# Performance work log

Hardware: AMD Instinct MI355X
Metric: run time of the kernel (lower is better)

The kernel has to match this reference:

```python
import jax, jax.numpy as jnp
import numpy as np

NUM_EXPERTS = 8
TOP_K = 2
HIDDEN = 1024
NUM_TOKENS = 8192


def setup_inputs() -> dict:
    key = jax.random.key(0)
    k1, k2, k3 = jax.random.split(key, 3)
    x = jax.random.normal(k1, (NUM_TOKENS, HIDDEN), dtype=jnp.float32)
    # gate: nn.Linear(hidden, num_experts, bias=False) -> weight [E, H]
    gate_w = jax.random.normal(k2, (NUM_EXPERTS, HIDDEN), dtype=jnp.float32) * 0.02
    # experts: nn.Linear(hidden, hidden, bias=False) stacked -> [E, H_out, H_in]
    expert_w = jax.random.normal(k3, (NUM_EXPERTS, HIDDEN, HIDDEN), dtype=jnp.float32) * 0.02
    return {"x": x, "gate_w": gate_w, "expert_w": expert_w}


def reference(x, gate_w, expert_w):
    # --- routing ---
    logits = jnp.einsum("th,eh->te", x, gate_w)          # [T, E]
    probs = jax.nn.softmax(logits, axis=-1)
    weights, indices = jax.lax.top_k(probs, TOP_K)        # [T, K], [T, K]

    # --- expert compute (equivalent of dispatch + per-expert GEMM) ---
    # y_e = x @ W_e^T for every expert; tokens then gather their top-k rows.
    all_y = jnp.einsum("td,ehd->eth", x, expert_w)        # [E, T, H]

    # --- weighted combine (gather by routed expert ids) ---
    t_idx = jnp.arange(x.shape[0])[None, :]               # [1, T]
    y_sel = all_y[indices.T, t_idx, :]                    # [K, T, H]
    out = jnp.einsum("tk,kth->th", weights, y_sel)        # [T, H]
    return out
```

## Files before the change

### kernel.cpp

```cpp
#include <hip/hip_runtime.h>
#include <hip/hip_bf16.h>
#include <stdint.h>

#define NUM_TOKENS 8192
#define HIDDEN 1024
#define NEXP 8
#define TOPK 2

typedef __bf16 bf16;
typedef __bf16 bf16x4 __attribute__((ext_vector_type(4)));
typedef __bf16 bf16x8 __attribute__((ext_vector_type(8)));
typedef float f32x4 __attribute__((ext_vector_type(4)));

__device__ __forceinline__ void gld_lds16(const void* g, void* l) {
  __builtin_amdgcn_global_load_lds(
      (const __attribute__((address_space(1))) void*)(uintptr_t)g,
      (__attribute__((address_space(3))) void*)(uint32_t)(uintptr_t)l,
      16, 0, 0);
}

__global__ __launch_bounds__(256) void gate_route_kernel(
    const float* __restrict__ x, const float* __restrict__ gw,
    bf16* __restrict__ xbf, int* __restrict__ echoice, float* __restrict__ pchoice)
{
  const int wid  = threadIdx.x >> 6;
  const int lane = threadIdx.x & 63;
  const int t = blockIdx.x * 4 + wid;

  const float* xrow = x + (size_t)t * HIDDEN;
  bf16* xbrow = xbf + (size_t)t * HIDDEN;

  float acc[NEXP];
#pragma unroll
  for (int e = 0; e < NEXP; ++e) acc[e] = 0.f;

#pragma unroll
  for (int it = 0; it < 4; ++it) {
    const int idx = it * 256 + lane * 4;
    float4 xv = *(const float4*)(xrow + idx);
    bf16x4 xb;
    xb[0] = (bf16)xv.x; xb[1] = (bf16)xv.y; xb[2] = (bf16)xv.z; xb[3] = (bf16)xv.w;
    *(bf16x4*)(xbrow + idx) = xb;
#pragma unroll
    for (int e = 0; e < NEXP; ++e) {
      float4 gv = *(const float4*)(gw + e * HIDDEN + idx);
      acc[e] += xv.x * gv.x + xv.y * gv.y + xv.z * gv.z + xv.w * gv.w;
    }
  }
#pragma unroll
  for (int e = 0; e < NEXP; ++e) {
#pragma unroll
    for (int off = 32; off > 0; off >>= 1)
      acc[e] += __shfl_xor(acc[e], off, 64);
  }

  if (lane == 0) {
    float m = acc[0];
#pragma unroll
    for (int e = 1; e < NEXP; ++e) m = fmaxf(m, acc[e]);
    float p[NEXP]; float s = 0.f;
#pragma unroll
    for (int e = 0; e < NEXP; ++e) { p[e] = expf(acc[e] - m); s += p[e]; }
    const float inv = 1.f / s;
#pragma unroll
    for (int e = 0; e < NEXP; ++e) p[e] *= inv;
    int i0 = 0; float p0 = p[0];
#pragma unroll
    for (int e = 1; e < NEXP; ++e) if (p[e] > p0) { p0 = p[e]; i0 = e; }
    int i1 = -1; float p1 = -1.f;
#pragma unroll
    for (int e = 0; e < NEXP; ++e) if (e != i0 && p[e] > p1) { p1 = p[e]; i1 = e; }

    echoice[t]              = i0;
    echoice[NUM_TOKENS + t] = i1;
    pchoice[t]              = p0;
    pchoice[NUM_TOKENS + t] = p1;
  }
}

__global__ __launch_bounds__(1024) void build_lists_kernel(
    const int* __restrict__ echoice, const float* __restrict__ pchoice,
    int* __restrict__ cnt, int* __restrict__ tok, float* __restrict__ wt)
{
  const int tid  = threadIdx.x;
  const int wave = tid >> 6;
  const int lane = tid & 63;
  const int k = wave >> 3;
  const int w = wave & 7;
  const int tbase = w * 1024;

  const int*   ec = echoice + k * NUM_TOKENS;
  const float* pc = pchoice + k * NUM_TOKENS;

  __shared__ int wcnt[2][8][NEXP];
  __shared__ int woff[2][8][NEXP];

  const unsigned long long lower = ((unsigned long long)1 << lane) - 1;

  int   ev[16];
  float pv[16];
#pragma unroll
  for (int c = 0; c < 16; ++c) {
    ev[c] = ec[tbase + c * 64 + lane];
    pv[c] = pc[tbase + c * 64 + lane];
  }

  int cl[NEXP];
#pragma unroll
  for (int e = 0; e < NEXP; ++e) cl[e] = 0;
#pragma unroll
  for (int c = 0; c < 16; ++c) {
#pragma unroll
    for (int l = 0; l < NEXP; ++l)
      cl[l] += __popcll(__ballot(ev[c] == l));
  }
  if (lane < NEXP) wcnt[k][w][lane] = cl[lane];
  __syncthreads();

  if (lane < NEXP) {
    int off = 0;
#pragma unroll
    for (int ww = 0; ww < 8; ++ww) {
      if (ww == w) woff[k][w][lane] = off;
      off += wcnt[k][ww][lane];
    }
    if (w == 0) cnt[k * NEXP + lane] = off;
  }
  __syncthreads();

  int run[NEXP];
#pragma unroll
  for (int e = 0; e < NEXP; ++e) run[e] = woff[k][w][e];
#pragma unroll
  for (int c = 0; c < 16; ++c) {
    const int e = ev[c];
    int pos = 0;
#pragma unroll
    for (int l = 0; l < NEXP; ++l) {
      const unsigned long long m = __ballot(ev[c] == l);
      if (e == l) pos = run[l] + __popcll(m & lower);
      run[l] += __popcll(m);
    }
    const int list = k * NEXP + e;
    tok[(size_t)list * NUM_TOKENS + pos] = tbase + c * 64 + lane;
    wt [(size_t)list * NUM_TOKENS + pos] = pv[c];
  }
}

__global__ __launch_bounds__(256) void convert_w_kernel(
    const float* __restrict__ w, bf16* __restrict__ wbf)
{
  const size_t i = ((size_t)blockIdx.x * 256 + threadIdx.x) * 4;
  float4 v = *(const float4*)(w + i);
  bf16x4 b;
  b[0] = (bf16)v.x; b[1] = (bf16)v.y; b[2] = (bf16)v.z; b[3] = (bf16)v.w;
  *(bf16x4*)(wbf + i) = b;
}

template <int PASS>
__global__ __launch_bounds__(256) void moe_gemm_kernel(
    const bf16* __restrict__ xbf, const bf16* __restrict__ wbf,
    const int* __restrict__ cnt, const int* __restrict__ tok,
    const float* __restrict__ wt, float* __restrict__ out)
{
  const int e  = blockIdx.z;
  const int mt = blockIdx.y;
  const int nt = blockIdx.x;
  const int list = PASS * NEXP + e;
  const int count = cnt[list];
  const int m0 = mt * 128;
  if (m0 >= count) return;
  const int rows = min(128, count - m0);

  __shared__ __align__(16) bf16 As[128 * 32];
  __shared__ __align__(16) bf16 Bs[128 * 32];
  __shared__ int   tok_s[128];
  __shared__ float wt_s[128];

  const int tid = threadIdx.x;
  if (tid < 128) {
    if (tid < rows) {
      tok_s[tid] = tok[(size_t)list * NUM_TOKENS + m0 + tid];
      wt_s[tid]  = wt [(size_t)list * NUM_TOKENS + m0 + tid];
    } else { tok_s[tid] = 0; wt_s[tid] = 0.f; }
  }
  __syncthreads();

  const int rr = tid >> 2;
  const int c8 = tid & 3;
  const bf16* gA0 = xbf + (size_t)tok_s[rr] * HIDDEN + c8 * 8;
  const bf16* gA1 = xbf + (size_t)tok_s[64 + rr] * HIDDEN + c8 * 8;
  const bf16* gB0 = wbf + (size_t)e * HIDDEN * HIDDEN
                  + (size_t)(nt * 128 + rr) * HIDDEN + c8 * 8;
  const bf16* gB1 = gB0 + (size_t)64 * HIDDEN;
  bf16* lA = As + tid * 8;
  bf16* lB = Bs + tid * 8;

  const int wid  = tid >> 6;
  const int lane = tid & 63;
  const int wm = (wid >> 1) * 64;
  const int wn = (wid & 1) * 64;
  const int qm = lane & 15;
  const int q8 = (lane >> 4) * 8;

  f32x4 acc[4][4];
#pragma unroll
  for (int i = 0; i < 4; ++i)
#pragma unroll
    for (int j = 0; j < 4; ++j) acc[i][j] = (f32x4){0.f, 0.f, 0.f, 0.f};

  for (int kc = 0; kc < HIDDEN; kc += 32) {
    gld_lds16(gA0 + kc, lA);
    gld_lds16(gA1 + kc, lA + 64 * 32);
    gld_lds16(gB0 + kc, lB);
    gld_lds16(gB1 + kc, lB + 64 * 32);
    __syncthreads();

    bf16x8 a[4], b[4];
#pragma unroll
    for (int i = 0; i < 4; ++i)
      a[i] = *(const bf16x8*)(As + (wm + i * 16 + qm) * 32 + q8);
#pragma unroll
    for (int j = 0; j < 4; ++j)
      b[j] = *(const bf16x8*)(Bs + (wn + j * 16 + qm) * 32 + q8);
#pragma unroll
    for (int i = 0; i < 4; ++i)
#pragma unroll
      for (int j = 0; j < 4; ++j)
        acc[i][j] = __builtin_amdgcn_mfma_f32_16x16x32_bf16(a[i], b[j], acc[i][j], 0, 0, 0);
    __syncthreads();
  }

  const int h0 = nt * 128 + wn + (lane & 15);
#pragma unroll
  for (int i = 0; i < 4; ++i) {
    const int rbase = wm + i * 16 + (lane >> 4) * 4;
#pragma unroll
    for (int r = 0; r < 4; ++r) {
      const int rl = rbase + r;
      if (rl < rows) {
        const int t = tok_s[rl];
        const float w = wt_s[rl];
        float* orow = out + (size_t)t * HIDDEN + h0;
#pragma unroll
        for (int j = 0; j < 4; ++j) {
          const float v = w * acc[i][j][r];
          if (PASS == 0) orow[j * 16] = v;
          else           orow[j * 16] += v;
        }
      }
    }
  }
}

extern "C" void kernel_launch(void* const* d_in, const int* in_sizes, int n_in,
                              void* d_out, int out_size, void* d_ws, size_t ws_size,
                              hipStream_t stream) {
  const float* x  = (const float*)d_in[0];
  const float* gw = (const float*)d_in[1];
  const float* ew = (const float*)d_in[2];
  float* out = (float*)d_out;

  char* ws = (char*)d_ws;
  int*   cnt     = (int*)ws;
  int*   echoice = (int*)(ws + 256);
  float* pchoice = (float*)(ws + 256 + (size_t)2 * NUM_TOKENS * 4);
  int*   tok = (int*)(ws + 256 + (size_t)4 * NUM_TOKENS * 4);
  float* wt  = (float*)(ws + 256 + (size_t)20 * NUM_TOKENS * 4);
  bf16*  xbf = (bf16*)(ws + 256 + (size_t)36 * NUM_TOKENS * 4);
  bf16*  wbf = (bf16*)((char*)xbf + (size_t)NUM_TOKENS * HIDDEN * 2);

  gate_route_kernel<<<NUM_TOKENS / 4, 256, 0, stream>>>(x, gw, xbf, echoice, pchoice);
  build_lists_kernel<<<1, 1024, 0, stream>>>(echoice, pchoice, cnt, tok, wt);
  convert_w_kernel<<<(NEXP * HIDDEN * HIDDEN) / (4 * 256), 256, 0, stream>>>(ew, wbf);

  dim3 grid(HIDDEN / 128, NUM_TOKENS / 128, NEXP);
  moe_gemm_kernel<0><<<grid, 256, 0, stream>>>(xbf, wbf, cnt, tok, wt, out);
  moe_gemm_kernel<1><<<grid, 256, 0, stream>>>(xbf, wbf, cnt, tok, wt, out);
}
```

Baseline: 213.1 us.

## Swizzle LDS tiles and remap GEMM block IDs for XCD-aware L2 reuse

Adds an XOR swizzle to the 16-byte chunk placement in the A/B shared-memory tiles so MFMA fragment reads hit fewer LDS bank conflicts. The 3D grid is flattened to 1D and block IDs are remapped so that all 8 N-tiles of one (expert, M-tile) pair run on the same XCD. That XCD can then reuse the gathered token rows in its L2. Empty M-tiles still launch and exit early, and the index math ties the grid to fixed sizes.

```diff
diff --git a/kernel.cpp b/kernel.cpp
--- a/kernel.cpp
+++ b/kernel.cpp
@@ -163,9 +163,14 @@
     const int* __restrict__ cnt, const int* __restrict__ tok,
     const float* __restrict__ wt, float* __restrict__ out)
 {
-  const int e  = blockIdx.z;
-  const int mt = blockIdx.y;
-  const int nt = blockIdx.x;
+  const int id   = blockIdx.x;
+  const int xcd  = id & 7;
+  const int rr_  = id >> 3;
+  const int nt   = rr_ & 7;
+  const int pair = (rr_ >> 3) * 8 + xcd;
+  const int e    = pair >> 6;
+  const int mt   = pair & 63;
+
   const int list = PASS * NEXP + e;
   const int count = cnt[list];
   const int m0 = mt * 128;
@@ -186,12 +191,13 @@
   }
   __syncthreads();
 
-  const int rr = tid >> 2;
-  const int c8 = tid & 3;
-  const bf16* gA0 = xbf + (size_t)tok_s[rr] * HIDDEN + c8 * 8;
-  const bf16* gA1 = xbf + (size_t)tok_s[64 + rr] * HIDDEN + c8 * 8;
+  const int rr    = tid >> 2;
+  const int cslot = tid & 3;
+  const int c     = cslot ^ (rr & 3);
+  const bf16* gA0 = xbf + (size_t)tok_s[rr] * HIDDEN + c * 8;
+  const bf16* gA1 = xbf + (size_t)tok_s[64 + rr] * HIDDEN + c * 8;
   const bf16* gB0 = wbf + (size_t)e * HIDDEN * HIDDEN
-                  + (size_t)(nt * 128 + rr) * HIDDEN + c8 * 8;
+                  + (size_t)(nt * 128 + rr) * HIDDEN + c * 8;
   const bf16* gB1 = gB0 + (size_t)64 * HIDDEN;
   bf16* lA = As + tid * 8;
   bf16* lB = Bs + tid * 8;
@@ -201,7 +207,7 @@
   const int wm = (wid >> 1) * 64;
   const int wn = (wid & 1) * 64;
   const int qm = lane & 15;
-  const int q8 = (lane >> 4) * 8;
+  const int cx = ((lane >> 4) ^ (qm & 3)) * 8;
 
   f32x4 acc[4][4];
 #pragma unroll
@@ -219,10 +225,10 @@
     bf16x8 a[4], b[4];
 #pragma unroll
     for (int i = 0; i < 4; ++i)
-      a[i] = *(const bf16x8*)(As + (wm + i * 16 + qm) * 32 + q8);
+      a[i] = *(const bf16x8*)(As + (wm + i * 16 + qm) * 32 + cx);
 #pragma unroll
     for (int j = 0; j < 4; ++j)
-      b[j] = *(const bf16x8*)(Bs + (wn + j * 16 + qm) * 32 + q8);
+      b[j] = *(const bf16x8*)(Bs + (wn + j * 16 + qm) * 32 + cx);
 #pragma unroll
     for (int i = 0; i < 4; ++i)
 #pragma unroll
@@ -274,7 +280,6 @@
   build_lists_kernel<<<1, 1024, 0, stream>>>(echoice, pchoice, cnt, tok, wt);
   convert_w_kernel<<<(NEXP * HIDDEN * HIDDEN) / (4 * 256), 256, 0, stream>>>(ew, wbf);
 
-  dim3 grid(HIDDEN / 128, NUM_TOKENS / 128, NEXP);
-  moe_gemm_kernel<0><<<grid, 256, 0, stream>>>(xbf, wbf, cnt, tok, wt, out);
-  moe_gemm_kernel<1><<<grid, 256, 0, stream>>>(xbf, wbf, cnt, tok, wt, out);
-}
+  moe_gemm_kernel<0><<<4096, 256, 0, stream>>>(xbf, wbf, cnt, tok, wt, out);
+  moe_gemm_kernel<1><<<4096, 256, 0, stream>>>(xbf, wbf, cnt, tok, wt, out);
+}
```

Result: slower. 220.5 us (+3.5%).
